# Kernel optimization log

Hardware: AMD Instinct MI355X
Metric: run time of the kernel (lower is better)

Reference implementation:

```python
import jax, jax.numpy as jnp
import numpy as np

B, T, DIN, DOUT = 2, 2048, 1024, 1024
G, H = 4, 16
HPG = H // G          # heads per group = 4
DH = DOUT // H        # head dim = 64
THETA = 10000.0


def _rope_tables(t, dh):
    inv_freq = 1.0 / (THETA ** (np.arange(0, dh, 2, dtype=np.float32) / dh))
    pos = np.arange(t, dtype=np.float32)
    freqs = np.outer(pos, inv_freq)              # [T, DH/2]
    emb = np.concatenate([freqs, freqs], axis=-1)  # [T, DH]
    return jnp.asarray(np.cos(emb)), jnp.asarray(np.sin(emb))


def _rotate_half(x):
    x1, x2 = jnp.split(x, 2, axis=-1)
    return jnp.concatenate([-x2, x1], axis=-1)


def setup_inputs() -> dict:
    key = jax.random.key(0)
    ks = jax.random.split(key, 5)
    s = 0.02
    x = jax.random.normal(ks[0], (B, T, DIN), jnp.float32)
    Wq = jax.random.normal(ks[1], (DIN, DOUT), jnp.float32) * s
    Wk = jax.random.normal(ks[2], (DIN, G * DH), jnp.float32) * s
    Wv = jax.random.normal(ks[3], (DIN, G * DH), jnp.float32) * s
    Wo = jax.random.normal(ks[4], (DOUT, DOUT), jnp.float32) * s
    cos, sin = _rope_tables(T, DH)
    return {"x": x, "Wq": Wq, "Wk": Wk, "Wv": Wv, "Wo": Wo, "cos": cos, "sin": sin}


def reference(x, Wq, Wk, Wv, Wo, cos, sin):
    b, t, _ = x.shape
    # projections
    q = (x @ Wq).reshape(b, t, G, HPG, DH).transpose(0, 2, 1, 3, 4)  # [B,G,T,Hpg,DH]
    k = (x @ Wk).reshape(b, t, G, DH).transpose(0, 2, 1, 3)           # [B,G,T,DH]
    v = (x @ Wv).reshape(b, t, G, DH).transpose(0, 2, 1, 3)           # [B,G,T,DH]
    # RoPE (cos/sin [T,DH]; for q broadcast over Hpg via extra axis)
    q = q * cos[:, None, :] + _rotate_half(q) * sin[:, None, :]
    k = k * cos + _rotate_half(k) * sin
    q = q.transpose(0, 1, 3, 2, 4)  # [B,G,Hpg,T,DH]
    # scores [B,G,Hpg,T,T]
    scores = jnp.einsum('bghtd,bgsd->bghts', q, k)
    causal = jnp.triu(jnp.ones((t, t), bool), k=1)
    scores = jnp.where(causal, -jnp.inf, scores)
    # NOTE: original code divides by sqrt(token_len), not sqrt(head_dim)
    attn = jax.nn.softmax(scores / jnp.float32(t) ** 0.5, axis=-1)
    out = jnp.einsum('bghts,bgsd->bghtd', attn, v)     # [B,G,Hpg,T,DH]
    out = out.transpose(0, 3, 1, 2, 4).reshape(b, t, DOUT)
    return out @ Wo
```

## Files before the change

kernel.cpp:

```cpp
#include <hip/hip_runtime.h>
#include <hip/hip_bf16.h>

typedef __attribute__((ext_vector_type(8))) short short8;
typedef __attribute__((ext_vector_type(4))) float f32x4;
typedef __attribute__((ext_vector_type(16))) float f32x16;

#define T_    2048
#define QKVN  1536
#define DOUT_ 1024

__device__ __forceinline__ unsigned short bf16r(float f) {
    union { float f; unsigned u; } v; v.f = f;
    unsigned r = v.u + 0x7fffu + ((v.u >> 16) & 1u);
    return (unsigned short)(r >> 16);
}
__device__ __forceinline__ float fbf16(short s) {
    union { unsigned u; float f; } v; v.u = ((unsigned)(unsigned short)s) << 16;
    return v.f;
}
__device__ __forceinline__ void plswap(unsigned &a, unsigned &b) {
    asm volatile("v_permlane32_swap_b32 %0, %1" : "+v"(a), "+v"(b));
}
__device__ __forceinline__ unsigned cvtpk(float lo, float hi) {
    unsigned r;
    asm("v_cvt_pk_bf16_f32 %0, %1, %2" : "=v"(r) : "v"(lo), "v"(hi));
    return r;
}
__device__ __forceinline__ void gload_lds16(const void* g, void* l) {
    __builtin_amdgcn_global_load_lds(
        (const __attribute__((address_space(1))) void*)g,
        (__attribute__((address_space(3))) void*)l, 16, 0, 0);
}

__global__ __launch_bounds__(256)
void k_xbf(const float* __restrict__ src, short* __restrict__ dst, int n8) {
    int i = blockIdx.x * blockDim.x + threadIdx.x;
    if (i >= n8) return;
    const float* s = src + (size_t)i * 8;
    float4 f1 = *(const float4*)s;
    float4 f2 = *(const float4*)(s + 4);
    uint4 o;
    o.x = (unsigned)bf16r(f1.x) | ((unsigned)bf16r(f1.y) << 16);
    o.y = (unsigned)bf16r(f1.z) | ((unsigned)bf16r(f1.w) << 16);
    o.z = (unsigned)bf16r(f2.x) | ((unsigned)bf16r(f2.y) << 16);
    o.w = (unsigned)bf16r(f2.z) | ((unsigned)bf16r(f2.w) << 16);
    *(uint4*)(dst + (size_t)i * 8) = o;
}

__global__ __launch_bounds__(256)
void k_transpose(const float* __restrict__ src, short* __restrict__ dst,
                 int K, int N) {
    __shared__ short tile[64][72];
    int tk = blockIdx.x * 64;
    int tn = blockIdx.y * 64;
    int t = threadIdx.x;
    int r4 = t >> 6, c = t & 63;
#pragma unroll
    for (int i = 0; i < 16; i++) {
        int row = i * 4 + r4;
        tile[c][row] = (short)bf16r(src[(size_t)(tk + row) * N + tn + c]);
    }
    __syncthreads();
    int row = t >> 2, seg = t & 3;
    short8 a = *(const short8*)&tile[row][seg * 16];
    short8 b = *(const short8*)&tile[row][seg * 16 + 8];
    *(short8*)&dst[(size_t)(tn + row) * K + tk + seg * 16]     = a;
    *(short8*)&dst[(size_t)(tn + row) * K + tk + seg * 16 + 8] = b;
}

__global__ __launch_bounds__(256)
void k_vt(const short* __restrict__ qkv, short* __restrict__ vt) {
    __shared__ short tile[64][72];
    int bid = blockIdx.x;
    int b = bid & 1, g = (bid >> 1) & 3, tt = bid >> 3;
    int t0v = tt * 64;
    int tid = threadIdx.x;
    int row = tid >> 2, sp = tid & 3;
    const short* src = qkv + ((size_t)(b * T_ + t0v + row) * QKVN + 1280 + g * 64 + sp * 16);
    uint4 a = *(const uint4*)src;
    uint4 c2 = *(const uint4*)(src + 8);
    const short* ap = (const short*)&a;
    const short* cp = (const short*)&c2;
#pragma unroll
    for (int x = 0; x < 8; x++) tile[sp * 16 + x][row]     = ap[x];
#pragma unroll
    for (int x = 0; x < 8; x++) tile[sp * 16 + 8 + x][row] = cp[x];
    __syncthreads();
    int d = tid >> 2;
    short* dst = vt + ((size_t)((b * 4 + g) * 64 + d) * T_ + t0v + sp * 16);
    *(uint4*)dst       = *(const uint4*)&tile[d][sp * 16];
    *(uint4*)(dst + 8) = *(const uint4*)&tile[d][sp * 16 + 8];
}

template <int CF32, int ROPE>
__global__ __launch_bounds__(256, 4)
void k_gemm(const short* __restrict__ A, const short* __restrict__ Bt,
            void* __restrict__ Cv, int M, int N, int K,
            const float* __restrict__ cosT, const float* __restrict__ sinT) {
    __shared__ __align__(16) short As[64][64];
    __shared__ __align__(16) short Bs[128][64];
    int tid = threadIdx.x;
    int l = tid & 63, w = tid >> 6;
    int lr = l & 15, lg = l >> 4;
    int m0 = blockIdx.x * 64;
    int n0 = blockIdx.y * 128;
    int wr = (w >> 1) * 32, wc = (w & 1) * 64;
    int lrow = l >> 3, lcol = (l & 7) * 8;

    f32x4 z = {0.f, 0.f, 0.f, 0.f};
    f32x4 acc[2][4];
#pragma unroll
    for (int m = 0; m < 2; m++)
#pragma unroll
        for (int n = 0; n < 4; n++) acc[m][n] = z;

    for (int k0 = 0; k0 < K; k0 += 64) {
#pragma unroll
        for (int i = 0; i < 2; i++) {
            int ch = w * 2 + i;
            gload_lds16(A + (size_t)(m0 + ch * 8 + lrow) * K + k0 + lcol,
                        &As[ch * 8][0]);
        }
#pragma unroll
        for (int i = 0; i < 4; i++) {
            int ch = w * 4 + i;
            gload_lds16(Bt + (size_t)(n0 + ch * 8 + lrow) * K + k0 + lcol,
                        &Bs[ch * 8][0]);
        }
        __syncthreads();
#pragma unroll
        for (int kk = 0; kk < 2; kk++) {
            short8 af[2], bf[4];
#pragma unroll
            for (int m = 0; m < 2; m++)
                af[m] = *(const short8*)&As[wr + m * 16 + lr][kk * 32 + lg * 8];
#pragma unroll
            for (int n = 0; n < 4; n++)
                bf[n] = *(const short8*)&Bs[wc + n * 16 + lr][kk * 32 + lg * 8];
#pragma unroll
            for (int m = 0; m < 2; m++)
#pragma unroll
                for (int n = 0; n < 4; n++)
                    acc[m][n] = __builtin_amdgcn_mfma_f32_16x16x32_bf16(
                        af[m], bf[n], acc[m][n], 0, 0, 0);
        }
        __syncthreads();
    }
#pragma unroll
    for (int m = 0; m < 2; m++)
#pragma unroll
        for (int r = 0; r < 4; r++) {
            int row = m0 + wr + m * 16 + lg * 4 + r;
            if (ROPE) {
                int h = (n0 + wc) >> 6;
                if (h < 20) {
                    int t = row & (T_ - 1);
#pragma unroll
                    for (int n = 0; n < 2; n++) {
                        int d = n * 16 + lr;
                        float cd = cosT[t * 64 + d];
                        float sd = sinT[t * 64 + d];
                        float a = acc[m][n][r], bb = acc[m][n + 2][r];
                        acc[m][n][r]     = a * cd - bb * sd;
                        acc[m][n + 2][r] = bb * cd + a * sd;
                    }
                }
            }
#pragma unroll
            for (int n = 0; n < 4; n++) {
                int col = n0 + wc + n * 16 + lr;
                float v = acc[m][n][r];
                if (CF32) ((float*)Cv)[(size_t)row * N + col] = v;
                else      ((short*)Cv)[(size_t)row * N + col] = (short)bf16r(v);
            }
        }
}

__global__ __launch_bounds__(256, 4)
void k_attn(const short* __restrict__ qkv, const short* __restrict__ vt,
            short* __restrict__ opart, float* __restrict__ lpart) {
    __shared__ __align__(16) short Ks[64][72];
    __shared__ __align__(16) short Vs[64][72];
    int id = blockIdx.x;
    int bg = id & 7;
    int vv = 159 - (id >> 3);
    int qt, c, nc;
    if (vv < 64) { qt = vv >> 1; c = vv & 1; nc = 2; }
    else { int v2 = vv - 64; qt = 32 + (v2 & 31); c = v2 >> 5; nc = 3; }
    int slot = bg * 160 + vv;
    int b = bg & 1, g = (bg >> 1) & 3;
    int q0 = qt * 32;
    int nt = (qt + 2) >> 1;
    int t0 = c * nt / nc, t1 = (c + 1) * nt / nc;

    int tid = threadIdx.x;
    int w = tid >> 6;
    int l = tid & 63;
    int lc = l & 31, hi = l >> 5;
    const float s2 = 0.03187928f;
    size_t rowbase = (size_t)b * T_ * QKVN;
    int qcol = g * 256 + w * 64;
    int kcol = 1024 + g * 64;
    const short* vbase = vt + (size_t)((b * 4 + g) * 64) * T_;

    short8 qf[4];
#pragma unroll
    for (int dkk = 0; dkk < 4; dkk++) {
        short8 raw = *(const short8*)(qkv + rowbase + (size_t)(q0 + lc) * QKVN
                                      + qcol + dkk * 16 + hi * 8);
        short8 sc;
#pragma unroll
        for (int x = 0; x < 8; x++) sc[x] = (short)bf16r(fbf16(raw[x]) * s2);
        qf[dkk] = sc;
    }

    int srow = tid >> 2, sseg = tid & 3;
    uint4 sK0, sK1, sV0, sV1;
    auto STAGE_LOAD = [&](int kt) {
        int s0 = kt * 64;
        const short* kp = qkv + rowbase + (size_t)(s0 + srow) * QKVN + kcol + sseg * 16;
        sK0 = *(const uint4*)kp; sK1 = *(const uint4*)(kp + 8);
        const short* vp = vbase + (size_t)srow * T_ + s0 + sseg * 16;
        sV0 = *(const uint4*)vp; sV1 = *(const uint4*)(vp + 8);
    };
    auto STAGE_WRITE = [&]() {
        *(uint4*)&Ks[srow][sseg * 16]     = sK0;
        *(uint4*)&Ks[srow][sseg * 16 + 8] = sK1;
        *(uint4*)&Vs[srow][sseg * 16]     = sV0;
        *(uint4*)&Vs[srow][sseg * 16 + 8] = sV1;
    };

    f32x16 Z16 = {0.f,0.f,0.f,0.f,0.f,0.f,0.f,0.f,0.f,0.f,0.f,0.f,0.f,0.f,0.f,0.f};
    f32x16 acc[2];
    acc[0] = Z16; acc[1] = Z16;
    float lp = 0.f;

    if (t0 < t1) STAGE_LOAD(t0);
    for (int kt = t0; kt < t1; kt++) {
        int s0 = kt * 64;
        bool last = (kt == nt - 1);
        __syncthreads();
        STAGE_WRITE();
        __syncthreads();
        if (kt + 1 < t1) STAGE_LOAD(kt + 1);

#pragma unroll
        for (int kf = 0; kf < 2; kf++) {
            f32x16 s = Z16;
            __builtin_amdgcn_s_setprio(1);
#pragma unroll
            for (int dkk = 0; dkk < 4; dkk++) {
                short8 ka = *(const short8*)&Ks[kf * 32 + lc][dkk * 16 + hi * 8];
                s = __builtin_amdgcn_mfma_f32_32x32x16_bf16(ka, qf[dkk], s, 0, 0, 0);
            }
            __builtin_amdgcn_s_setprio(0);
            float p[16];
            if (last) {
                int qrow = q0 + lc;
                int kb = s0 + kf * 32 + hi * 4;
#pragma unroll
                for (int reg = 0; reg < 16; reg++) {
                    int key = kb + (reg & 3) + ((reg >> 2) << 3);
                    p[reg] = (key <= qrow) ? exp2f(s[reg]) : 0.f;
                }
            } else {
#pragma unroll
                for (int reg = 0; reg < 16; reg++) p[reg] = exp2f(s[reg]);
            }
#pragma unroll
            for (int reg = 0; reg < 16; reg++) lp += p[reg];
            unsigned pk[4][2];
#pragma unroll
            for (int sb = 0; sb < 4; sb++) {
                pk[sb][0] = cvtpk(p[4 * sb],     p[4 * sb + 1]);
                pk[sb][1] = cvtpk(p[4 * sb + 2], p[4 * sb + 3]);
            }
            __builtin_amdgcn_s_setprio(1);
#pragma unroll
            for (int kk = 0; kk < 2; kk++) {
                unsigned a0 = pk[2 * kk][0], b0 = pk[2 * kk + 1][0];
                unsigned a1 = pk[2 * kk][1], b1 = pk[2 * kk + 1][1];
                plswap(a0, b0);
                plswap(a1, b1);
                union { unsigned u[4]; short8 s8; } pb;
                pb.u[0] = a0; pb.u[1] = a1; pb.u[2] = b0; pb.u[3] = b1;
#pragma unroll
                for (int df = 0; df < 2; df++) {
                    short8 va = *(const short8*)&Vs[df * 32 + lc][kf * 32 + kk * 16 + hi * 8];
                    acc[df] = __builtin_amdgcn_mfma_f32_32x32x16_bf16(va, pb.s8, acc[df], 0, 0, 0);
                }
            }
            __builtin_amdgcn_s_setprio(0);
        }
    }

    float lt = lp + __shfl_xor(lp, 32, 64);

    short* ob = opart + (size_t)slot * 8192 + lc * 256 + w * 64;
#pragma unroll
    for (int df = 0; df < 2; df++)
#pragma unroll
        for (int sb = 0; sb < 4; sb++) {
            unsigned u0 = cvtpk(acc[df][4 * sb],     acc[df][4 * sb + 1]);
            unsigned u1 = cvtpk(acc[df][4 * sb + 2], acc[df][4 * sb + 3]);
            uint2 uv = {u0, u1};
            *(uint2*)(ob + df * 32 + sb * 8 + hi * 4) = uv;
        }
    if (hi == 0) lpart[slot * 128 + lc * 4 + w] = lt;
}

__global__ __launch_bounds__(256)
void k_comb(const short* __restrict__ opart, const float* __restrict__ lpart,
            short* __restrict__ attn) {
    int id = blockIdx.x;
    int bg = id & 7, qt = id >> 3;
    int b = bg & 1, g = (bg >> 1) & 3;
    int t = threadIdx.x;
    int row = t >> 3, s = t & 7;
    int head = s >> 1, colseg = s * 32;
    int nc = (qt < 32) ? 2 : 3;
    float acc[32];
#pragma unroll
    for (int i = 0; i < 32; i++) acc[i] = 0.f;
    float lsum = 0.f;
    for (int c = 0; c < nc; c++) {
        int vv = (qt < 32) ? (2 * qt + c) : (64 + (qt - 32) + 32 * c);
        int oid = bg * 160 + vv;
        lsum += lpart[oid * 128 + row * 4 + head];
        const short* ob = opart + (size_t)oid * 8192 + row * 256 + colseg;
#pragma unroll
        for (int i = 0; i < 4; i++) {
            uint4 v = *(const uint4*)(ob + i * 8);
            const short* vs = (const short*)&v;
#pragma unroll
            for (int j = 0; j < 8; j++) acc[i * 8 + j] += fbf16(vs[j]);
        }
    }
    float inv = 1.0f / lsum;
    unsigned out[16];
#pragma unroll
    for (int i = 0; i < 16; i++)
        out[i] = cvtpk(acc[2 * i] * inv, acc[2 * i + 1] * inv);
    short* dst = attn + ((size_t)(b * T_ + qt * 32 + row)) * DOUT_ + g * 256 + colseg;
#pragma unroll
    for (int i = 0; i < 4; i++) *(uint4*)(dst + i * 8) = *(const uint4*)&out[i * 4];
}

extern "C" void kernel_launch(void* const* d_in, const int* in_sizes, int n_in,
                              void* d_out, int out_size, void* d_ws, size_t ws_size,
                              hipStream_t stream) {
    const float* x    = (const float*)d_in[0];
    const float* Wq   = (const float*)d_in[1];
    const float* Wk   = (const float*)d_in[2];
    const float* Wv   = (const float*)d_in[3];
    const float* Wo   = (const float*)d_in[4];
    const float* cosT = (const float*)d_in[5];
    const float* sinT = (const float*)d_in[6];

    char* ws = (char*)d_ws;
    short* WT    = (short*)(ws);
    short* WoT   = (short*)(ws + 3145728);
    short* QKV   = (short*)(ws + 5242880);
    short* ATT   = (short*)(ws + 17825792);
    short* VT    = (short*)(ws + 26214400);
    short* XB    = (short*)(ws + 28311552);
    short* OPART = (short*)(ws + 28311552);
    float* LPART = (float*)(ws + 49283072);

    k_xbf<<<2048, 256, 0, stream>>>(x, XB, 524288);
    k_transpose<<<dim3(16, 16), 256, 0, stream>>>(Wq, WT, 1024, 1024);
    k_transpose<<<dim3(16, 4),  256, 0, stream>>>(Wk, WT + 1024 * 1024, 1024, 256);
    k_transpose<<<dim3(16, 4),  256, 0, stream>>>(Wv, WT + 1280 * 1024, 1024, 256);
    k_transpose<<<dim3(16, 16), 256, 0, stream>>>(Wo, WoT, 1024, 1024);

    k_gemm<0, 1><<<dim3(64, 12), 256, 0, stream>>>(XB, WT, (void*)QKV,
                                                   4096, 1536, 1024, cosT, sinT);
    k_vt<<<256, 256, 0, stream>>>(QKV, VT);
    k_attn<<<1280, 256, 0, stream>>>(QKV, VT, OPART, LPART);
    k_comb<<<512, 256, 0, stream>>>(OPART, LPART, ATT);
    k_gemm<1, 0><<<dim3(64, 8), 256, 0, stream>>>(ATT, WoT, d_out,
                                                  4096, 1024, 1024, nullptr, nullptr);
}
```

Baseline: 114.8 us.

## Double-buffer attention K/V tiles with direct global-to-LDS loads and XOR swizzle

Replaces the register-staged, padded single-buffer K/V tiles in the attention kernel with two LDS buffers filled by direct global-to-LDS loads. The next tile now streams into the alternate buffer while the current one is consumed, so one of the two per-iteration barriers goes away. An XOR swizzle on 16-byte chunks replaces the row padding to avoid bank conflicts. This costs more LDS per block, and correctness depends on the async LDS loads being waited on before the barrier.

```diff
diff --git a/kernel.cpp b/kernel.cpp
--- a/kernel.cpp
+++ b/kernel.cpp
@@ -179,8 +179,8 @@
 __global__ __launch_bounds__(256, 4)
 void k_attn(const short* __restrict__ qkv, const short* __restrict__ vt,
             short* __restrict__ opart, float* __restrict__ lpart) {
-    __shared__ __align__(16) short Ks[64][72];
-    __shared__ __align__(16) short Vs[64][72];
+    __shared__ __align__(16) short KsL[2][4096];
+    __shared__ __align__(16) short VsL[2][4096];
     int id = blockIdx.x;
     int bg = id & 7;
     int vv = 159 - (id >> 3);
@@ -214,20 +214,24 @@
         qf[dkk] = sc;
     }
 
-    int srow = tid >> 2, sseg = tid & 3;
-    uint4 sK0, sK1, sV0, sV1;
-    auto STAGE_LOAD = [&](int kt) {
+    auto STAGE = [&](int kt, int bu) {
         int s0 = kt * 64;
-        const short* kp = qkv + rowbase + (size_t)(s0 + srow) * QKVN + kcol + sseg * 16;
-        sK0 = *(const uint4*)kp; sK1 = *(const uint4*)(kp + 8);
-        const short* vp = vbase + (size_t)srow * T_ + s0 + sseg * 16;
-        sV0 = *(const uint4*)vp; sV1 = *(const uint4*)(vp + 8);
-    };
-    auto STAGE_WRITE = [&]() {
-        *(uint4*)&Ks[srow][sseg * 16]     = sK0;
-        *(uint4*)&Ks[srow][sseg * 16 + 8] = sK1;
-        *(uint4*)&Vs[srow][sseg * 16]     = sV0;
-        *(uint4*)&Vs[srow][sseg * 16 + 8] = sV1;
+#pragma unroll
+        for (int i = 0; i < 2; i++) {
+            int C = ((w * 2 + i) << 6) + l;
+            int r = C >> 3;
+            int jj = (C & 7) ^ (r & 7);
+            gload_lds16(qkv + rowbase + (size_t)(s0 + r) * QKVN + kcol + jj * 8,
+                        &KsL[bu][(w * 2 + i) * 512]);
+        }
+#pragma unroll
+        for (int i = 0; i < 2; i++) {
+            int C = ((w * 2 + i) << 6) + l;
+            int r = C >> 3;
+            int jj = (C & 7) ^ (r & 7);
+            gload_lds16(vbase + (size_t)r * T_ + s0 + jj * 8,
+                        &VsL[bu][(w * 2 + i) * 512]);
+        }
     };
 
     f32x16 Z16 = {0.f,0.f,0.f,0.f,0.f,0.f,0.f,0.f,0.f,0.f,0.f,0.f,0.f,0.f,0.f,0.f};
@@ -235,14 +239,13 @@
     acc[0] = Z16; acc[1] = Z16;
     float lp = 0.f;
 
-    if (t0 < t1) STAGE_LOAD(t0);
+    if (t0 < t1) STAGE(t0, 0);
     for (int kt = t0; kt < t1; kt++) {
+        int bu = (kt - t0) & 1;
         int s0 = kt * 64;
         bool last = (kt == nt - 1);
         __syncthreads();
-        STAGE_WRITE();
-        __syncthreads();
-        if (kt + 1 < t1) STAGE_LOAD(kt + 1);
+        if (kt + 1 < t1) STAGE(kt + 1, bu ^ 1);
 
 #pragma unroll
         for (int kf = 0; kf < 2; kf++) {
@@ -250,7 +253,9 @@
             __builtin_amdgcn_s_setprio(1);
 #pragma unroll
             for (int dkk = 0; dkk < 4; dkk++) {
-                short8 ka = *(const short8*)&Ks[kf * 32 + lc][dkk * 16 + hi * 8];
+                int r = kf * 32 + lc;
+                int jd = dkk * 2 + hi;
+                short8 ka = *(const short8*)&KsL[bu][r * 64 + ((jd ^ (r & 7)) << 3)];
                 s = __builtin_amdgcn_mfma_f32_32x32x16_bf16(ka, qf[dkk], s, 0, 0, 0);
             }
             __builtin_amdgcn_s_setprio(0);
@@ -286,7 +291,9 @@
                 pb.u[0] = a0; pb.u[1] = a1; pb.u[2] = b0; pb.u[3] = b1;
 #pragma unroll
                 for (int df = 0; df < 2; df++) {
-                    short8 va = *(const short8*)&Vs[df * 32 + lc][kf * 32 + kk * 16 + hi * 8];
+                    int r = df * 32 + lc;
+                    int jk = kf * 4 + kk * 2 + hi;
+                    short8 va = *(const short8*)&VsL[bu][r * 64 + ((jk ^ (r & 7)) << 3)];
                     acc[df] = __builtin_amdgcn_mfma_f32_32x32x16_bf16(va, pb.s8, acc[df], 0, 0, 0);
                 }
             }
```

New measurement: 113.9 us. No clear change (-0.7%).
